# Optimization experiments

Measured on AMD Instinct MI355X. Metric: run time of the kernel, lower is better.

The kernel has to match this reference:

```python
import jax, jax.numpy as jnp
import numpy as np

N_NODES = 100000
N_EDGES = 3200000
N_GRAPHS = 256
IN_CH = 8
HID = 64


def _gcn_conv(x, W, b, src, dst, n):
    # PyG GCNConv default: add self-loops, symmetric normalization.
    # out_i = sum_{j->i} d_i^-1/2 d_j^-1/2 (xW)_j + (1/d_i)(xW)_i + b
    xw = x @ W                                     # [N, out]
    deg = jax.ops.segment_sum(jnp.ones_like(dst, dtype=xw.dtype), dst,
                              num_segments=n) + 1.0  # +1 for self-loop
    dinv = jax.lax.rsqrt(deg)
    norm = dinv[src] * dinv[dst]                   # [E]
    agg = jax.ops.segment_sum(xw[src] * norm[:, None], dst, num_segments=n)
    agg = agg + xw * (1.0 / deg)[:, None]          # self-loop term (norm = 1/deg)
    return agg + b


def setup_inputs() -> dict:
    key = jax.random.key(0)
    ks = jax.random.split(key, 12)
    x = jax.random.normal(ks[0], (N_NODES, IN_CH), dtype=jnp.float32)
    edge_index = jax.random.randint(ks[1], (2, N_EDGES), 0, N_NODES, dtype=jnp.int64)
    batch = jnp.sort(jax.random.randint(ks[2], (N_NODES,), 0, N_GRAPHS, dtype=jnp.int64))

    def glorot(k, fan_in, fan_out):
        s = jnp.sqrt(2.0 / (fan_in + fan_out)).astype(jnp.float32)
        return jax.random.normal(k, (fan_in, fan_out), dtype=jnp.float32) * s

    return {
        "x": x, "edge_index": edge_index, "batch": batch,
        "W1": glorot(ks[3], IN_CH, HID), "b1": jnp.zeros((HID,), jnp.float32),
        "W2": glorot(ks[4], HID, 2 * HID), "b2": jnp.zeros((2 * HID,), jnp.float32),
        "W3": glorot(ks[5], 2 * HID, HID), "b3": jnp.zeros((HID,), jnp.float32),
        "Wl1": glorot(ks[6], HID, HID // 2), "bl1": jnp.zeros((HID // 2,), jnp.float32),
        "Wl2": glorot(ks[7], HID // 2, 1), "bl2": jnp.zeros((1,), jnp.float32),
    }


def reference(x, edge_index, batch, W1, b1, W2, b2, W3, b3, Wl1, bl1, Wl2, bl2):
    src, dst = edge_index[0], edge_index[1]
    h = jax.nn.relu(_gcn_conv(x, W1, b1, src, dst, N_NODES))
    h = jax.nn.relu(_gcn_conv(h, W2, b2, src, dst, N_NODES))
    h = jax.nn.relu(_gcn_conv(h, W3, b3, src, dst, N_NODES))
    # global mean pool over graphs
    sums = jax.ops.segment_sum(h, batch, num_segments=N_GRAPHS)
    cnts = jax.ops.segment_sum(jnp.ones((N_NODES,), h.dtype), batch, num_segments=N_GRAPHS)
    g = sums / jnp.maximum(cnts, 1.0)[:, None]     # [G, HID]
    g = jax.nn.relu(g @ Wl1 + bl1)
    out = g @ Wl2 + bl2                            # [G, 1]
    return out[:, 0]
```

## Files before the change

### kernel.cpp

```cpp
#include <hip/hip_runtime.h>
#include <hip/hip_bf16.h>

#define N_NODES 100000
#define N_EDGES 3200000
#define N_GRAPHS 256
#define NB_BUCKETS 196
#define BSHIFT 9
#define NBLK 256
#define SCAN_BLKS 49
#define CSR_CAP 22528

#define OFF_SUMS      0u
#define OFF_CNTF      65536u
#define ZERO_BYTES    66560u
#define OFF_HIST      66560u
#define OFF_BSUM      267264u
#define OFF_ROWPTR    267776u
#define OFF_DINV      668160u
#define OFF_COL       1068544u
#define OFF_XS1       13868544u
#define OFF_BUFQ      20268544u
#define OFF_BUFR      45868544u
#define OFF_BUFP      71468544u
#define OFF_PAIRS     OFF_BUFP

__device__ __forceinline__ unsigned short f2bf(float f) {
    unsigned u = __float_as_uint(f);
    return (unsigned short)((u + 0x7fffu + ((u >> 16) & 1u)) >> 16);
}

__device__ __forceinline__ void acc_bf8(uint4 v, float m, float* a) {
    a[0] += m * __uint_as_float(v.x << 16);
    a[1] += m * __uint_as_float(v.x & 0xffff0000u);
    a[2] += m * __uint_as_float(v.y << 16);
    a[3] += m * __uint_as_float(v.y & 0xffff0000u);
    a[4] += m * __uint_as_float(v.z << 16);
    a[5] += m * __uint_as_float(v.z & 0xffff0000u);
    a[6] += m * __uint_as_float(v.w << 16);
    a[7] += m * __uint_as_float(v.w & 0xffff0000u);
}

__global__ __launch_bounds__(256) void hist_kernel(const int* __restrict__ dst,
                                                   int* __restrict__ hist,
                                                   int* __restrict__ zbase,
                                                   int E, int epb) {
    __shared__ int h[NB_BUCKETS];
    int t = threadIdx.x, blk = blockIdx.x;
    int gid = blk * 256 + t;
    if (gid < (int)(ZERO_BYTES / 4)) zbase[gid] = 0;
    if (t < NB_BUCKETS) h[t] = 0;
    __syncthreads();
    int e0 = blk * epb, e1 = min(e0 + epb, E);
    for (int e = e0 + t; e < e1; e += 256)
        atomicAdd(&h[__builtin_nontemporal_load(&dst[e]) >> BSHIFT], 1);
    __syncthreads();
    if (t < NB_BUCKETS) hist[t * NBLK + blk] = h[t];
}

__global__ __launch_bounds__(1024) void scanhA_kernel(int* __restrict__ hist,
                                                      int* __restrict__ bsum) {
    __shared__ int s[1024];
    int t = threadIdx.x;
    int i = blockIdx.x * 1024 + t;
    int v = hist[i];
    s[t] = v;
    __syncthreads();
    for (int off = 1; off < 1024; off <<= 1) {
        int add = (t >= off) ? s[t - off] : 0;
        __syncthreads();
        s[t] += add;
        __syncthreads();
    }
    hist[i] = s[t] - v;
    if (t == 1023) bsum[blockIdx.x] = s[t];
}

__global__ __launch_bounds__(256) void bin_kernel(const int* __restrict__ src,
                                                  const int* __restrict__ dst,
                                                  const int* __restrict__ hist,
                                                  const int* __restrict__ bsum,
                                                  int* __restrict__ packed, int E, int epb) {
    __shared__ int cur[NB_BUCKETS];
    __shared__ int boffL[SCAN_BLKS];
    int t = threadIdx.x, blk = blockIdx.x;
    if (t < 64) {
        int orig = (t < SCAN_BLKS) ? bsum[t] : 0;
        int v = orig;
        for (int off = 1; off < 64; off <<= 1) {
            int up = __shfl_up(v, off);
            if (t >= off) v += up;
        }
        if (t < SCAN_BLKS) boffL[t] = v - orig;
    }
    __syncthreads();
    if (t < NB_BUCKETS) {
        int i = t * NBLK + blk;
        cur[t] = hist[i] + boffL[i >> 10];
    }
    __syncthreads();
    int e0 = blk * epb, e1 = min(e0 + epb, E);
    for (int e = e0 + t; e < e1; e += 256) {
        int d = __builtin_nontemporal_load(&dst[e]);
        int sv = __builtin_nontemporal_load(&src[e]);
        int pos = atomicAdd(&cur[d >> BSHIFT], 1);
        packed[pos] = ((d & 511) << 17) | sv;
    }
}

__global__ __launch_bounds__(512) void csr_kernel(const int* __restrict__ packed,
                                                  const int* __restrict__ hist,
                                                  const int* __restrict__ bsum,
                                                  const float* __restrict__ x,
                                                  int* __restrict__ row_ptr,
                                                  float* __restrict__ dinv,
                                                  float* __restrict__ xs1,
                                                  int* __restrict__ col, int E) {
    __shared__ int cntL[512];
    __shared__ int rsL[512];
    __shared__ int fillL[512];
    __shared__ int boffL[SCAN_BLKS];
    __shared__ int srcL[CSR_CAP];
    int t = threadIdx.x, b = blockIdx.x;
    int lo = b << BSHIFT;
    int nloc = min(512, N_NODES - lo);
    cntL[t] = 0;
    fillL[t] = 0;
    if (t < 64) {
        int orig = (t < SCAN_BLKS) ? bsum[t] : 0;
        int v = orig;
        for (int off = 1; off < 64; off <<= 1) {
            int up = __shfl_up(v, off);
            if (t >= off) v += up;
        }
        if (t < SCAN_BLKS) boffL[t] = v - orig;
    }
    __syncthreads();
    int i0 = b * NBLK;
    int start = hist[i0] + boffL[i0 >> 10];
    int end;
    if (b == NB_BUCKETS - 1) end = E;
    else {
        int i1 = (b + 1) * NBLK;
        end = hist[i1] + boffL[i1 >> 10];
    }
    for (int e = start + t; e < end; e += 512)
        atomicAdd(&cntL[packed[e] >> 17], 1);
    __syncthreads();
    int v = cntL[t];
    __syncthreads();
    for (int off = 1; off < 512; off <<= 1) {
        int add = (t >= off) ? cntL[t - off] : 0;
        __syncthreads();
        cntL[t] += add;
        __syncthreads();
    }
    int rowstart = start + cntL[t] - v;
    rsL[t] = rowstart;
    if (t < nloc) {
        int node = lo + t;
        row_ptr[node] = rowstart;
        float d = rsqrtf((float)(v + 1));
        dinv[node] = d;
        const float4* xv = reinterpret_cast<const float4*>(x) + node * 2;
        float4 xa = xv[0], xb = xv[1];
        xa.x *= d; xa.y *= d; xa.z *= d; xa.w *= d;
        xb.x *= d; xb.y *= d; xb.z *= d; xb.w *= d;
        float4* xo = reinterpret_cast<float4*>(xs1) + node * 2;
        xo[0] = xa; xo[1] = xb;
    }
    if (b == NB_BUCKETS - 1 && t == 0) row_ptr[N_NODES] = E;
    __syncthreads();
    for (int e = start + t; e < end; e += 512) {
        int p = packed[e];
        int dl = p >> 17;
        int pos = rsL[dl] + atomicAdd(&fillL[dl], 1);
        int rel = pos - start;
        if (rel < CSR_CAP) srcL[rel] = p & 0x1FFFF;
        else col[pos] = p & 0x1FFFF;
    }
    __syncthreads();
    int lim = min(end - start, CSR_CAP);
    for (int i = t; i < lim; i += 512)
        col[start + i] = srcL[i];
}

__global__ __launch_bounds__(256) void agg8g1_kernel(
        const float* __restrict__ xs, const int* __restrict__ row_ptr,
        const int* __restrict__ col, const float* __restrict__ dinv,
        const float* __restrict__ W1, const float* __restrict__ b1,
        unsigned short* __restrict__ xs2, int n) {
    int wave = threadIdx.x >> 6;
    int node = blockIdx.x * 4 + wave;
    if (node >= n) return;
    int lane = threadIdx.x & 63;
    int j = lane >> 1, l = lane & 1;
    int e0 = row_ptr[node], e1 = row_ptr[node + 1];
    float4 acc0 = {0.f, 0.f, 0.f, 0.f}, acc1 = acc0;
    if (j == 0) {
        const float4 sv = *reinterpret_cast<const float4*>(&xs[node * 8 + 4 * l]);
        acc0.x += sv.x; acc0.y += sv.y; acc0.z += sv.z; acc0.w += sv.w;
    }
    int base = e0;
    for (; base + 64 <= e1; base += 64) {
        int s0 = __builtin_nontemporal_load(&col[base + j]);
        int s1 = __builtin_nontemporal_load(&col[base + 32 + j]);
        const float4 v0 = *reinterpret_cast<const float4*>(&xs[s0 * 8 + 4 * l]);
        const float4 v1 = *reinterpret_cast<const float4*>(&xs[s1 * 8 + 4 * l]);
        acc0.x += v0.x; acc0.y += v0.y; acc0.z += v0.z; acc0.w += v0.w;
        acc1.x += v1.x; acc1.y += v1.y; acc1.z += v1.z; acc1.w += v1.w;
    }
    if (base < e1) {
        int ee0 = base + j;
        int ee1 = base + 32 + j;
        int s0 = __builtin_nontemporal_load(&col[min(ee0, e1 - 1)]);
        int s1 = __builtin_nontemporal_load(&col[min(ee1, e1 - 1)]);
        float m0 = (ee0 < e1) ? 1.0f : 0.0f;
        float m1 = (ee1 < e1) ? 1.0f : 0.0f;
        const float4 v0 = *reinterpret_cast<const float4*>(&xs[s0 * 8 + 4 * l]);
        const float4 v1 = *reinterpret_cast<const float4*>(&xs[s1 * 8 + 4 * l]);
        acc0.x += m0 * v0.x; acc0.y += m0 * v0.y; acc0.z += m0 * v0.z; acc0.w += m0 * v0.w;
        acc1.x += m1 * v1.x; acc1.y += m1 * v1.y; acc1.z += m1 * v1.z; acc1.w += m1 * v1.w;
    }
    float4 r;
    r.x = acc0.x + acc1.x; r.y = acc0.y + acc1.y;
    r.z = acc0.z + acc1.z; r.w = acc0.w + acc1.w;
    r.x += __shfl_xor(r.x, 2);  r.y += __shfl_xor(r.y, 2);
    r.z += __shfl_xor(r.z, 2);  r.w += __shfl_xor(r.w, 2);
    r.x += __shfl_xor(r.x, 4);  r.y += __shfl_xor(r.y, 4);
    r.z += __shfl_xor(r.z, 4);  r.w += __shfl_xor(r.w, 4);
    r.x += __shfl_xor(r.x, 8);  r.y += __shfl_xor(r.y, 8);
    r.z += __shfl_xor(r.z, 8);  r.w += __shfl_xor(r.w, 8);
    r.x += __shfl_xor(r.x, 16); r.y += __shfl_xor(r.y, 16);
    r.z += __shfl_xor(r.z, 16); r.w += __shfl_xor(r.w, 16);
    r.x += __shfl_xor(r.x, 32); r.y += __shfl_xor(r.y, 32);
    r.z += __shfl_xor(r.z, 32); r.w += __shfl_xor(r.w, 32);
    float d = dinv[node];
    r.x *= d; r.y *= d; r.z *= d; r.w *= d;
    float z10 = __shfl(r.x, 0), z11 = __shfl(r.y, 0);
    float z12 = __shfl(r.z, 0), z13 = __shfl(r.w, 0);
    float z14 = __shfl(r.x, 1), z15 = __shfl(r.y, 1);
    float z16 = __shfl(r.z, 1), z17 = __shfl(r.w, 1);
    float a = b1[lane];
    a += z10 * W1[0 * 64 + lane];
    a += z11 * W1[1 * 64 + lane];
    a += z12 * W1[2 * 64 + lane];
    a += z13 * W1[3 * 64 + lane];
    a += z14 * W1[4 * 64 + lane];
    a += z15 * W1[5 * 64 + lane];
    a += z16 * W1[6 * 64 + lane];
    a += z17 * W1[7 * 64 + lane];
    xs2[node * 64 + lane] = f2bf(d * fmaxf(a, 0.0f));
}

__global__ __launch_bounds__(256) void agg64bf_kernel(
        const unsigned short* __restrict__ xs, const int* __restrict__ row_ptr,
        const int* __restrict__ col, const float* __restrict__ dinv,
        float* __restrict__ z, int n) {
    int wave = threadIdx.x >> 6;
    int node = blockIdx.x * 4 + wave;
    if (node >= n) return;
    int lane = threadIdx.x & 63;
    int j = lane >> 3, l = lane & 7;
    int e0 = row_ptr[node], e1 = row_ptr[node + 1];
    float a[8] = {0.f, 0.f, 0.f, 0.f, 0.f, 0.f, 0.f, 0.f};
    uint4 sv = *reinterpret_cast<const uint4*>(&xs[node * 64 + 8 * l]);
    int base = e0;
    for (; e1 - base > 48; base += 32) {
        int s0 = __builtin_nontemporal_load(&col[base + j]);
        int s1 = __builtin_nontemporal_load(&col[base + 8 + j]);
        int s2 = __builtin_nontemporal_load(&col[base + 16 + j]);
        int s3 = __builtin_nontemporal_load(&col[base + 24 + j]);
        uint4 v0 = *reinterpret_cast<const uint4*>(&xs[s0 * 64 + 8 * l]);
        uint4 v1 = *reinterpret_cast<const uint4*>(&xs[s1 * 64 + 8 * l]);
        uint4 v2 = *reinterpret_cast<const uint4*>(&xs[s2 * 64 + 8 * l]);
        uint4 v3 = *reinterpret_cast<const uint4*>(&xs[s3 * 64 + 8 * l]);
        acc_bf8(v0, 1.f, a); acc_bf8(v1, 1.f, a);
        acc_bf8(v2, 1.f, a); acc_bf8(v3, 1.f, a);
    }
    int rem = e1 - base;
    if (rem > 0) {
        int e1m1 = e1 - 1;
        bool g4 = rem > 32, g5 = rem > 40;
        int i0 = base + j,      i1 = base + 8 + j;
        int i2 = base + 16 + j, i3 = base + 24 + j;
        int i4 = base + 32 + j, i5 = base + 40 + j;
        int c0 = __builtin_nontemporal_load(&col[min(i0, e1m1)]);
        int c1 = __builtin_nontemporal_load(&col[min(i1, e1m1)]);
        int c2 = __builtin_nontemporal_load(&col[min(i2, e1m1)]);
        int c3 = __builtin_nontemporal_load(&col[min(i3, e1m1)]);
        int c4 = 0, c5 = 0;
        if (g4) c4 = __builtin_nontemporal_load(&col[min(i4, e1m1)]);
        if (g5) c5 = __builtin_nontemporal_load(&col[min(i5, e1m1)]);
        uint4 v0 = *reinterpret_cast<const uint4*>(&xs[c0 * 64 + 8 * l]);
        uint4 v1 = *reinterpret_cast<const uint4*>(&xs[c1 * 64 + 8 * l]);
        uint4 v2 = *reinterpret_cast<const uint4*>(&xs[c2 * 64 + 8 * l]);
        uint4 v3 = *reinterpret_cast<const uint4*>(&xs[c3 * 64 + 8 * l]);
        uint4 v4, v5;
        if (g4) v4 = *reinterpret_cast<const uint4*>(&xs[c4 * 64 + 8 * l]);
        if (g5) v5 = *reinterpret_cast<const uint4*>(&xs[c5 * 64 + 8 * l]);
        acc_bf8(v0, (i0 < e1) ? 1.f : 0.f, a);
        acc_bf8(v1, (i1 < e1) ? 1.f : 0.f, a);
        acc_bf8(v2, (i2 < e1) ? 1.f : 0.f, a);
        acc_bf8(v3, (i3 < e1) ? 1.f : 0.f, a);
        if (g4) acc_bf8(v4, (i4 < e1) ? 1.f : 0.f, a);
        if (g5) acc_bf8(v5, (i5 < e1) ? 1.f : 0.f, a);
    }
    acc_bf8(sv, (j == 0) ? 1.f : 0.f, a);
#pragma unroll
    for (int k = 0; k < 8; ++k) {
        a[k] += __shfl_xor(a[k], 8);
        a[k] += __shfl_xor(a[k], 16);
        a[k] += __shfl_xor(a[k], 32);
    }
    if (j == 0) {
        float d = dinv[node];
        float4 r0 = {a[0] * d, a[1] * d, a[2] * d, a[3] * d};
        float4 r1 = {a[4] * d, a[5] * d, a[6] * d, a[7] * d};
        *reinterpret_cast<float4*>(&z[node * 64 + 8 * l]) = r0;
        *reinterpret_cast<float4*>(&z[node * 64 + 8 * l + 4]) = r1;
    }
}

template <int K, int M, bool BIAS, bool RELU, bool SCALE, bool BF16OUT>
__global__ __launch_bounds__(256) void gemm_kernel(
        const float* __restrict__ X, const float* __restrict__ W,
        const float* __restrict__ b, const float* __restrict__ dinv,
        float* __restrict__ Y, int nrows) {
    constexpr int CG = M / 4;
    constexpr int RG = 256 / CG;
    constexpr int ROWS = RG * 4;
    constexpr int XSTR = K + 4;
    __shared__ float Wl[K * M];
    __shared__ float Xl[ROWS * XSTR];
    __shared__ float Bl[M];
    int tid = threadIdx.x;
    {
        const float4* Wv = reinterpret_cast<const float4*>(W);
        float4* Wlv = reinterpret_cast<float4*>(Wl);
        for (int i = tid; i < K * M / 4; i += 256) Wlv[i] = Wv[i];
    }
    if (tid < M) Bl[tid] = BIAS ? b[tid] : 0.0f;
    int cg = tid % CG;
    int rg = tid / CG;
    int ntiles = (nrows + ROWS - 1) / ROWS;
    for (int tile = blockIdx.x; tile < ntiles; tile += gridDim.x) {
        int row0 = tile * ROWS;
        __syncthreads();
        {
            int base4 = row0 * (K / 4);
            int tot4 = nrows * (K / 4);
            for (int i = tid; i < ROWS * K / 4; i += 256) {
                float4 v = {0.f, 0.f, 0.f, 0.f};
                if (base4 + i < tot4) v = reinterpret_cast<const float4*>(X)[base4 + i];
                int rr = i / (K / 4), kk = i % (K / 4);
                *reinterpret_cast<float4*>(&Xl[rr * XSTR + kk * 4]) = v;
            }
        }
        __syncthreads();
        float4 acc[4];
#pragma unroll
        for (int rr = 0; rr < 4; ++rr)
            acc[rr] = *reinterpret_cast<const float4*>(&Bl[cg * 4]);
#pragma unroll 1
        for (int k = 0; k < K; k += 4) {
            const float4 w0 = *reinterpret_cast<const float4*>(&Wl[(k + 0) * M + cg * 4]);
            const float4 w1 = *reinterpret_cast<const float4*>(&Wl[(k + 1) * M + cg * 4]);
            const float4 w2 = *reinterpret_cast<const float4*>(&Wl[(k + 2) * M + cg * 4]);
            const float4 w3 = *reinterpret_cast<const float4*>(&Wl[(k + 3) * M + cg * 4]);
#pragma unroll
            for (int rr = 0; rr < 4; ++rr) {
                const float4 xv = *reinterpret_cast<const float4*>(
                    &Xl[(rg * 4 + rr) * XSTR + k]);
                acc[rr].x += xv.x * w0.x + xv.y * w1.x + xv.z * w2.x + xv.w * w3.x;
                acc[rr].y += xv.x * w0.y + xv.y * w1.y + xv.z * w2.y + xv.w * w3.y;
                acc[rr].z += xv.x * w0.z + xv.y * w1.z + xv.z * w2.z + xv.w * w3.z;
                acc[rr].w += xv.x * w0.w + xv.y * w1.w + xv.z * w2.w + xv.w * w3.w;
            }
        }
#pragma unroll
        for (int rr = 0; rr < 4; ++rr) {
            int row = row0 + rg * 4 + rr;
            if (row < nrows) {
                float4 a = acc[rr];
                if constexpr (RELU) {
                    a.x = fmaxf(a.x, 0.f); a.y = fmaxf(a.y, 0.f);
                    a.z = fmaxf(a.z, 0.f); a.w = fmaxf(a.w, 0.f);
                }
                if constexpr (SCALE) {
                    float d = dinv[row];
                    a.x *= d; a.y *= d; a.z *= d; a.w *= d;
                }
                if constexpr (BF16OUT) {
                    unsigned short* Yh = reinterpret_cast<unsigned short*>(Y);
                    uint2 p;
                    p.x = (unsigned)f2bf(a.x) | ((unsigned)f2bf(a.y) << 16);
                    p.y = (unsigned)f2bf(a.z) | ((unsigned)f2bf(a.w) << 16);
                    *reinterpret_cast<uint2*>(&Yh[row * M + cg * 4]) = p;
                } else {
                    *reinterpret_cast<float4*>(&Y[row * M + cg * 4]) = a;
                }
            }
        }
    }
}

#define POOL_NPB 128
__global__ __launch_bounds__(256) void pool_kernel(
        const float* __restrict__ z3, const float* __restrict__ b3,
        const int* __restrict__ batch, float* __restrict__ sums,
        float* __restrict__ cntf, int n) {
    int wave = threadIdx.x >> 6;
    int lane = threadIdx.x & 63;
    int node0 = blockIdx.x * POOL_NPB + wave * 32;
    int nodeEnd = min(node0 + 32, n);
    if (node0 >= n) return;
    float bias = b3[lane];
    float acc = 0.0f, cnt = 0.0f;
    int curg = -1;
    for (int node = node0; node < nodeEnd; ++node) {
        int g = batch[node];
        if (g != curg) {
            if (curg >= 0) {
                atomicAdd(&sums[curg * 64 + lane], acc);
                if (lane == 0) atomicAdd(&cntf[curg], cnt);
            }
            curg = g; acc = 0.0f; cnt = 0.0f;
        }
        acc += fmaxf(__builtin_nontemporal_load(&z3[node * 64 + lane]) + bias, 0.0f);
        cnt += 1.0f;
    }
    if (curg >= 0) {
        atomicAdd(&sums[curg * 64 + lane], acc);
        if (lane == 0) atomicAdd(&cntf[curg], cnt);
    }
}

__global__ void mlp_kernel(const float* __restrict__ sums, const float* __restrict__ cntf,
                           const float* __restrict__ Wl1, const float* __restrict__ bl1,
                           const float* __restrict__ Wl2, const float* __restrict__ bl2,
                           float* __restrict__ out) {
    __shared__ float gv[64];
    __shared__ float hid[32];
    int g = blockIdx.x, t = threadIdx.x;
    float denom = fmaxf(cntf[g], 1.0f);
    gv[t] = sums[g * 64 + t] / denom;
    __syncthreads();
    if (t < 32) {
        float a = bl1[t];
#pragma unroll
        for (int k = 0; k < 64; ++k) a += gv[k] * Wl1[k * 32 + t];
        hid[t] = fmaxf(a, 0.0f);
    }
    __syncthreads();
    if (t == 0) {
        float o = bl2[0];
#pragma unroll
        for (int k = 0; k < 32; ++k) o += hid[k] * Wl2[k];
        out[g] = o;
    }
}

extern "C" void kernel_launch(void* const* d_in, const int* in_sizes, int n_in,
                              void* d_out, int out_size, void* d_ws, size_t ws_size,
                              hipStream_t stream) {
    const float* x   = (const float*)d_in[0];
    const int* ei    = (const int*)d_in[1];
    const int* batch = (const int*)d_in[2];
    const float* W1  = (const float*)d_in[3];
    const float* b1  = (const float*)d_in[4];
    const float* W2  = (const float*)d_in[5];
    const float* b2  = (const float*)d_in[6];
    const float* W3  = (const float*)d_in[7];
    const float* b3  = (const float*)d_in[8];
    const float* Wl1 = (const float*)d_in[9];
    const float* bl1 = (const float*)d_in[10];
    const float* Wl2 = (const float*)d_in[11];
    const float* bl2 = (const float*)d_in[12];
    float* out = (float*)d_out;

    const int N = N_NODES;
    const int E = in_sizes[1] / 2;
    const int* src = ei;
    const int* dst = ei + E;

    char* ws = (char*)d_ws;
    float* sums    = (float*)(ws + OFF_SUMS);
    float* cntf    = (float*)(ws + OFF_CNTF);
    int*   hist    = (int*)(ws + OFF_HIST);
    int*   bsum    = (int*)(ws + OFF_BSUM);
    int*   row_ptr = (int*)(ws + OFF_ROWPTR);
    float* dinv    = (float*)(ws + OFF_DINV);
    int*   col     = (int*)(ws + OFF_COL);
    float* xs1     = (float*)(ws + OFF_XS1);
    float* bufQ    = (float*)(ws + OFF_BUFQ);
    float* bufR    = (float*)(ws + OFF_BUFR);
    float* bufP    = (float*)(ws + OFF_BUFP);
    int*   packed  = (int*)(ws + OFF_PAIRS);

    int epb = (E + NBLK - 1) / NBLK;
    hist_kernel<<<NBLK, 256, 0, stream>>>(dst, hist, (int*)ws, E, epb);
    scanhA_kernel<<<SCAN_BLKS, 1024, 0, stream>>>(hist, bsum);
    bin_kernel<<<NBLK, 256, 0, stream>>>(src, dst, hist, bsum, packed, E, epb);
    csr_kernel<<<NB_BUCKETS, 512, 0, stream>>>(packed, hist, bsum, x,
                                               row_ptr, dinv, xs1, col, E);

    agg8g1_kernel<<<(N + 3) / 4, 256, 0, stream>>>(xs1, row_ptr, col, dinv, W1, b1,
                                                   (unsigned short*)bufQ, N);

    agg64bf_kernel<<<(N + 3) / 4, 256, 0, stream>>>((const unsigned short*)bufQ,
                                                    row_ptr, col, dinv, bufR, N);
    gemm_kernel<64, 128, true, true, false, false><<<3125, 256, 0, stream>>>(
        bufR, W2, b2, nullptr, bufP, N);

    gemm_kernel<128, 64, false, false, true, true><<<1563, 256, 0, stream>>>(
        bufP, W3, nullptr, dinv, bufR, N);
    agg64bf_kernel<<<(N + 3) / 4, 256, 0, stream>>>((const unsigned short*)bufR,
                                                    row_ptr, col, dinv, bufQ, N);

    pool_kernel<<<(N + POOL_NPB - 1) / POOL_NPB, 256, 0, stream>>>(bufQ, b3, batch, sums, cntf, N);
    mlp_kernel<<<N_GRAPHS, 64, 0, stream>>>(sums, cntf, Wl1, bl1, Wl2, bl2, out);
}
```

Before: 404.8 us.

## Stage binned edges in LDS per bucket before coalesced global writes

After: 418.6 us. 1.03x slower.

```diff
diff --git a/kernel.cpp b/kernel.cpp
--- a/kernel.cpp
+++ b/kernel.cpp
@@ -9,6 +9,8 @@
 #define NBLK 256
 #define SCAN_BLKS 49
 #define CSR_CAP 22528
+#define BIN_CAP 64
+#define BIN_CHUNK 6250
 
 #define OFF_SUMS      0u
 #define OFF_CNTF      65536u
@@ -80,8 +82,10 @@
                                                   const int* __restrict__ hist,
                                                   const int* __restrict__ bsum,
                                                   int* __restrict__ packed, int E, int epb) {
-    __shared__ int cur[NB_BUCKETS];
+    __shared__ int curL[NB_BUCKETS];
+    __shared__ int fillL[NB_BUCKETS];
     __shared__ int boffL[SCAN_BLKS];
+    __shared__ int buf[NB_BUCKETS * BIN_CAP];
     int t = threadIdx.x, blk = blockIdx.x;
     if (t < 64) {
         int orig = (t < SCAN_BLKS) ? bsum[t] : 0;
@@ -95,15 +99,38 @@
     __syncthreads();
     if (t < NB_BUCKETS) {
         int i = t * NBLK + blk;
-        cur[t] = hist[i] + boffL[i >> 10];
+        curL[t] = hist[i] + boffL[i >> 10];
+        fillL[t] = 0;
     }
     __syncthreads();
     int e0 = blk * epb, e1 = min(e0 + epb, E);
-    for (int e = e0 + t; e < e1; e += 256) {
-        int d = __builtin_nontemporal_load(&dst[e]);
-        int sv = __builtin_nontemporal_load(&src[e]);
-        int pos = atomicAdd(&cur[d >> BSHIFT], 1);
-        packed[pos] = ((d & 511) << 17) | sv;
+    for (int c0 = e0; c0 < e1; c0 += BIN_CHUNK) {
+        int c1 = min(c0 + BIN_CHUNK, e1);
+        for (int e = c0 + t; e < c1; e += 256) {
+            int d = __builtin_nontemporal_load(&dst[e]);
+            int sv = __builtin_nontemporal_load(&src[e]);
+            int b = d >> BSHIFT;
+            int val = ((d & 511) << 17) | sv;
+            int slot = atomicAdd(&fillL[b], 1);
+            if (slot < BIN_CAP) buf[b * BIN_CAP + slot] = val;
+            else packed[curL[b] + slot] = val;
+        }
+        __syncthreads();
+        {
+            int wave = t >> 6, lane = t & 63;
+            for (int b = wave; b < NB_BUCKETS; b += 4) {
+                int cnt = min(fillL[b], BIN_CAP);
+                int gp = curL[b];
+                for (int i = lane; i < cnt; i += 64)
+                    __builtin_nontemporal_store(buf[b * BIN_CAP + i], &packed[gp + i]);
+            }
+        }
+        __syncthreads();
+        if (t < NB_BUCKETS) {
+            curL[t] += fillL[t];
+            fillL[t] = 0;
+        }
+        __syncthreads();
     }
 }
 
```

## Store layer-1 input and intermediate activations in bf16 to cut traffic

Applied to the files above, without the earlier changes.

Result: no change. 405.9 us (+0.3%).

```diff
diff --git a/kernel.cpp b/kernel.cpp
--- a/kernel.cpp
+++ b/kernel.cpp
@@ -113,7 +113,7 @@
                                                   const float* __restrict__ x,
                                                   int* __restrict__ row_ptr,
                                                   float* __restrict__ dinv,
-                                                  float* __restrict__ xs1,
+                                                  unsigned short* __restrict__ xs1,
                                                   int* __restrict__ col, int E) {
     __shared__ int cntL[512];
     __shared__ int rsL[512];
@@ -163,10 +163,12 @@
         dinv[node] = d;
         const float4* xv = reinterpret_cast<const float4*>(x) + node * 2;
         float4 xa = xv[0], xb = xv[1];
-        xa.x *= d; xa.y *= d; xa.z *= d; xa.w *= d;
-        xb.x *= d; xb.y *= d; xb.z *= d; xb.w *= d;
-        float4* xo = reinterpret_cast<float4*>(xs1) + node * 2;
-        xo[0] = xa; xo[1] = xb;
+        uint4 p;
+        p.x = (unsigned)f2bf(xa.x * d) | ((unsigned)f2bf(xa.y * d) << 16);
+        p.y = (unsigned)f2bf(xa.z * d) | ((unsigned)f2bf(xa.w * d) << 16);
+        p.z = (unsigned)f2bf(xb.x * d) | ((unsigned)f2bf(xb.y * d) << 16);
+        p.w = (unsigned)f2bf(xb.z * d) | ((unsigned)f2bf(xb.w * d) << 16);
+        *reinterpret_cast<uint4*>(&xs1[node * 8]) = p;
     }
     if (b == NB_BUCKETS - 1 && t == 0) row_ptr[N_NODES] = E;
     __syncthreads();
@@ -185,7 +187,7 @@
 }
 
 __global__ __launch_bounds__(256) void agg8g1_kernel(
-        const float* __restrict__ xs, const int* __restrict__ row_ptr,
+        const unsigned short* __restrict__ xs, const int* __restrict__ row_ptr,
         const int* __restrict__ col, const float* __restrict__ dinv,
         const float* __restrict__ W1, const float* __restrict__ b1,
         unsigned short* __restrict__ xs2, int n) {
@@ -193,65 +195,44 @@
     int node = blockIdx.x * 4 + wave;
     if (node >= n) return;
     int lane = threadIdx.x & 63;
-    int j = lane >> 1, l = lane & 1;
+    float w[8];
+    float bias = b1[lane];
+#pragma unroll
+    for (int k = 0; k < 8; ++k) w[k] = W1[k * 64 + lane];
     int e0 = row_ptr[node], e1 = row_ptr[node + 1];
-    float4 acc0 = {0.f, 0.f, 0.f, 0.f}, acc1 = acc0;
-    if (j == 0) {
-        const float4 sv = *reinterpret_cast<const float4*>(&xs[node * 8 + 4 * l]);
-        acc0.x += sv.x; acc0.y += sv.y; acc0.z += sv.z; acc0.w += sv.w;
-    }
+    float a[8] = {0.f, 0.f, 0.f, 0.f, 0.f, 0.f, 0.f, 0.f};
+    uint4 sv = *reinterpret_cast<const uint4*>(&xs[node * 8]);
     int base = e0;
     for (; base + 64 <= e1; base += 64) {
-        int s0 = __builtin_nontemporal_load(&col[base + j]);
-        int s1 = __builtin_nontemporal_load(&col[base + 32 + j]);
-        const float4 v0 = *reinterpret_cast<const float4*>(&xs[s0 * 8 + 4 * l]);
-        const float4 v1 = *reinterpret_cast<const float4*>(&xs[s1 * 8 + 4 * l]);
-        acc0.x += v0.x; acc0.y += v0.y; acc0.z += v0.z; acc0.w += v0.w;
-        acc1.x += v1.x; acc1.y += v1.y; acc1.z += v1.z; acc1.w += v1.w;
+        int c = __builtin_nontemporal_load(&col[base + lane]);
+        uint4 v = *reinterpret_cast<const uint4*>(&xs[c * 8]);
+        acc_bf8(v, 1.f, a);
     }
     if (base < e1) {
-        int ee0 = base + j;
-        int ee1 = base + 32 + j;
-        int s0 = __builtin_nontemporal_load(&col[min(ee0, e1 - 1)]);
-        int s1 = __builtin_nontemporal_load(&col[min(ee1, e1 - 1)]);
-        float m0 = (ee0 < e1) ? 1.0f : 0.0f;
-        float m1 = (ee1 < e1) ? 1.0f : 0.0f;
-        const float4 v0 = *reinterpret_cast<const float4*>(&xs[s0 * 8 + 4 * l]);
-        const float4 v1 = *reinterpret_cast<const float4*>(&xs[s1 * 8 + 4 * l]);
-        acc0.x += m0 * v0.x; acc0.y += m0 * v0.y; acc0.z += m0 * v0.z; acc0.w += m0 * v0.w;
-        acc1.x += m1 * v1.x; acc1.y += m1 * v1.y; acc1.z += m1 * v1.z; acc1.w += m1 * v1.w;
-    }
-    float4 r;
-    r.x = acc0.x + acc1.x; r.y = acc0.y + acc1.y;
-    r.z = acc0.z + acc1.z; r.w = acc0.w + acc1.w;
-    r.x += __shfl_xor(r.x, 2);  r.y += __shfl_xor(r.y, 2);
-    r.z += __shfl_xor(r.z, 2);  r.w += __shfl_xor(r.w, 2);
-    r.x += __shfl_xor(r.x, 4);  r.y += __shfl_xor(r.y, 4);
-    r.z += __shfl_xor(r.z, 4);  r.w += __shfl_xor(r.w, 4);
-    r.x += __shfl_xor(r.x, 8);  r.y += __shfl_xor(r.y, 8);
-    r.z += __shfl_xor(r.z, 8);  r.w += __shfl_xor(r.w, 8);
-    r.x += __shfl_xor(r.x, 16); r.y += __shfl_xor(r.y, 16);
-    r.z += __shfl_xor(r.z, 16); r.w += __shfl_xor(r.w, 16);
-    r.x += __shfl_xor(r.x, 32); r.y += __shfl_xor(r.y, 32);
-    r.z += __shfl_xor(r.z, 32); r.w += __shfl_xor(r.w, 32);
+        int e = base + lane;
+        int c = __builtin_nontemporal_load(&col[min(e, e1 - 1)]);
+        uint4 v = *reinterpret_cast<const uint4*>(&xs[c * 8]);
+        acc_bf8(v, (e < e1) ? 1.f : 0.f, a);
+    }
+    acc_bf8(sv, (lane == 0) ? 1.f : 0.f, a);
+#pragma unroll
+    for (int k = 0; k < 8; ++k) {
+        a[k] += __shfl_xor(a[k], 1);
+        a[k] += __shfl_xor(a[k], 2);
+        a[k] += __shfl_xor(a[k], 4);
+    }
+    float v8 = a[lane & 7];
+    v8 += __shfl_xor(v8, 8);
+    v8 += __shfl_xor(v8, 16);
+    v8 += __shfl_xor(v8, 32);
     float d = dinv[node];
-    r.x *= d; r.y *= d; r.z *= d; r.w *= d;
-    float z10 = __shfl(r.x, 0), z11 = __shfl(r.y, 0);
-    float z12 = __shfl(r.z, 0), z13 = __shfl(r.w, 0);
-    float z14 = __shfl(r.x, 1), z15 = __shfl(r.y, 1);
-    float z16 = __shfl(r.z, 1), z17 = __shfl(r.w, 1);
-    float a = b1[lane];
-    a += z10 * W1[0 * 64 + lane];
-    a += z11 * W1[1 * 64 + lane];
-    a += z12 * W1[2 * 64 + lane];
-    a += z13 * W1[3 * 64 + lane];
-    a += z14 * W1[4 * 64 + lane];
-    a += z15 * W1[5 * 64 + lane];
-    a += z16 * W1[6 * 64 + lane];
-    a += z17 * W1[7 * 64 + lane];
-    xs2[node * 64 + lane] = f2bf(d * fmaxf(a, 0.0f));
-}
-
+    float acc = bias;
+#pragma unroll
+    for (int k = 0; k < 8; ++k) acc += (__shfl(v8, k) * d) * w[k];
+    xs2[node * 64 + lane] = f2bf(d * fmaxf(acc, 0.0f));
+}
+
+template <bool BF16OUT>
 __global__ __launch_bounds__(256) void agg64bf_kernel(
         const unsigned short* __restrict__ xs, const int* __restrict__ row_ptr,
         const int* __restrict__ col, const float* __restrict__ dinv,
@@ -314,14 +295,24 @@
     }
     if (j == 0) {
         float d = dinv[node];
-        float4 r0 = {a[0] * d, a[1] * d, a[2] * d, a[3] * d};
-        float4 r1 = {a[4] * d, a[5] * d, a[6] * d, a[7] * d};
-        *reinterpret_cast<float4*>(&z[node * 64 + 8 * l]) = r0;
-        *reinterpret_cast<float4*>(&z[node * 64 + 8 * l + 4]) = r1;
-    }
-}
-
-template <int K, int M, bool BIAS, bool RELU, bool SCALE, bool BF16OUT>
+        if constexpr (BF16OUT) {
+            unsigned short* zh = reinterpret_cast<unsigned short*>(z);
+            uint4 p;
+            p.x = (unsigned)f2bf(a[0] * d) | ((unsigned)f2bf(a[1] * d) << 16);
+            p.y = (unsigned)f2bf(a[2] * d) | ((unsigned)f2bf(a[3] * d) << 16);
+            p.z = (unsigned)f2bf(a[4] * d) | ((unsigned)f2bf(a[5] * d) << 16);
+            p.w = (unsigned)f2bf(a[6] * d) | ((unsigned)f2bf(a[7] * d) << 16);
+            *reinterpret_cast<uint4*>(&zh[node * 64 + 8 * l]) = p;
+        } else {
+            float4 r0 = {a[0] * d, a[1] * d, a[2] * d, a[3] * d};
+            float4 r1 = {a[4] * d, a[5] * d, a[6] * d, a[7] * d};
+            *reinterpret_cast<float4*>(&z[node * 64 + 8 * l]) = r0;
+            *reinterpret_cast<float4*>(&z[node * 64 + 8 * l + 4]) = r1;
+        }
+    }
+}
+
+template <int K, int M, bool BIAS, bool RELU, bool SCALE, bool BF16IN, bool BF16OUT>
 __global__ __launch_bounds__(256) void gemm_kernel(
         const float* __restrict__ X, const float* __restrict__ W,
         const float* __restrict__ b, const float* __restrict__ dinv,
@@ -351,7 +342,17 @@
             int tot4 = nrows * (K / 4);
             for (int i = tid; i < ROWS * K / 4; i += 256) {
                 float4 v = {0.f, 0.f, 0.f, 0.f};
-                if (base4 + i < tot4) v = reinterpret_cast<const float4*>(X)[base4 + i];
+                if (base4 + i < tot4) {
+                    if constexpr (BF16IN) {
+                        uint2 raw = reinterpret_cast<const uint2*>(X)[base4 + i];
+                        v.x = __uint_as_float(raw.x << 16);
+                        v.y = __uint_as_float(raw.x & 0xffff0000u);
+                        v.z = __uint_as_float(raw.y << 16);
+                        v.w = __uint_as_float(raw.y & 0xffff0000u);
+                    } else {
+                        v = reinterpret_cast<const float4*>(X)[base4 + i];
+                    }
+                }
                 int rr = i / (K / 4), kk = i % (K / 4);
                 *reinterpret_cast<float4*>(&Xl[rr * XSTR + kk * 4]) = v;
             }
@@ -491,7 +492,7 @@
     int*   row_ptr = (int*)(ws + OFF_ROWPTR);
     float* dinv    = (float*)(ws + OFF_DINV);
     int*   col     = (int*)(ws + OFF_COL);
-    float* xs1     = (float*)(ws + OFF_XS1);
+    unsigned short* xs1 = (unsigned short*)(ws + OFF_XS1);
     float* bufQ    = (float*)(ws + OFF_BUFQ);
     float* bufR    = (float*)(ws + OFF_BUFR);
     float* bufP    = (float*)(ws + OFF_BUFP);
@@ -507,15 +508,15 @@
     agg8g1_kernel<<<(N + 3) / 4, 256, 0, stream>>>(xs1, row_ptr, col, dinv, W1, b1,
                                                    (unsigned short*)bufQ, N);
 
-    agg64bf_kernel<<<(N + 3) / 4, 256, 0, stream>>>((const unsigned short*)bufQ,
-                                                    row_ptr, col, dinv, bufR, N);
-    gemm_kernel<64, 128, true, true, false, false><<<3125, 256, 0, stream>>>(
+    agg64bf_kernel<true><<<(N + 3) / 4, 256, 0, stream>>>(
+        (const unsigned short*)bufQ, row_ptr, col, dinv, bufR, N);
+    gemm_kernel<64, 128, true, true, false, true, true><<<3125, 256, 0, stream>>>(
         bufR, W2, b2, nullptr, bufP, N);
 
-    gemm_kernel<128, 64, false, false, true, true><<<1563, 256, 0, stream>>>(
+    gemm_kernel<128, 64, false, false, true, true, true><<<1563, 256, 0, stream>>>(
         bufP, W3, nullptr, dinv, bufR, N);
-    agg64bf_kernel<<<(N + 3) / 4, 256, 0, stream>>>((const unsigned short*)bufR,
-                                                    row_ptr, col, dinv, bufQ, N);
+    agg64bf_kernel<false><<<(N + 3) / 4, 256, 0, stream>>>(
+        (const unsigned short*)bufR, row_ptr, col, dinv, bufQ, N);
 
     pool_kernel<<<(N + POOL_NPB - 1) / POOL_NPB, 256, 0, stream>>>(bufQ, b3, batch, sums, cntf, N);
     mlp_kernel<<<N_GRAPHS, 64, 0, stream>>>(sums, cntf, Wl1, bl1, Wl2, bl2, out);
```
